# Kernel tuning notes

Hardware: AMD Instinct MI355X
Metric: run time of the kernel (lower is better)

## Reference

```python
import jax, jax.numpy as jnp
import numpy as np

N = 50000   # nodes
E = 800000  # edges per metapath
P = 3       # num_meta_paths
H = 4       # heads
D = 64      # out_size per head
IN = H * D  # in_size = 256 (required by residual g_emb.flatten(1) + h)
EPS = 1e-5
NEG_SLOPE = 0.2  # DGL GATConv leaky_relu default


def setup_inputs() -> dict:
    key = jax.random.key(0)
    ks = jax.random.split(key, 7)
    h = jax.random.normal(ks[0], (N, IN), jnp.float32)
    path_mask = jnp.ones((N, P), jnp.float32)
    src = jax.random.randint(ks[1], (P, E), 0, N, jnp.int32)
    dst = jax.random.randint(ks[2], (P, E), 0, N, jnp.int32)
    # per-metapath GATConv params (bias=False)
    fc_w = jax.random.normal(ks[3], (P, IN, H * D), jnp.float32) * 0.05
    attn_l = jax.random.normal(ks[4], (P, H, D), jnp.float32) * 0.05
    attn_r = jax.random.normal(ks[5], (P, H, D), jnp.float32) * 0.05
    bn_gamma = jnp.ones((IN,), jnp.float32)
    bn_beta = jnp.zeros((IN,), jnp.float32)
    return {"h": h, "path_mask": path_mask, "src": src, "dst": dst,
            "fc_w": fc_w, "attn_l": attn_l, "attn_r": attn_r,
            "bn_gamma": bn_gamma, "bn_beta": bn_beta}


def _gat(h, src, dst, w, al, ar):
    # DGL GATConv: linear proj, additive attention, edge-softmax over dst neighborhoods
    feat = (h @ w).reshape(N, H, D)                       # [N,H,D]
    el = jnp.sum(feat * al, axis=-1)                      # [N,H]
    er = jnp.sum(feat * ar, axis=-1)                      # [N,H]
    e = jax.nn.leaky_relu(el[src] + er[dst], NEG_SLOPE)   # [E,H]
    # numerically-stable segment softmax over incoming edges of each dst node
    m = jax.ops.segment_max(e, dst, num_segments=N)       # [N,H]
    ex = jnp.exp(e - m[dst])
    denom = jax.ops.segment_sum(ex, dst, num_segments=N)  # [N,H]
    alpha = ex / denom[dst]                               # [E,H]
    out = jax.ops.segment_sum(alpha[:, :, None] * feat[src], dst, num_segments=N)  # [N,H,D]
    return jax.nn.relu(out), alpha


def _bn(x, gamma, beta):
    # BatchNorm1d in training mode: batch statistics over node dim
    mu = jnp.mean(x, axis=0)
    var = jnp.var(x, axis=0)
    return gamma * (x - mu) * jax.lax.rsqrt(var + EPS) + beta


def reference(h, path_mask, src, dst, fc_w, attn_l, attn_r, bn_gamma, bn_beta):
    embs, attns = [], []
    for p in range(P):
        o, a = _gat(h, src[p], dst[p], fc_w[p], attn_l[p], attn_r[p])
        embs.append(_bn(o.reshape(N, H * D) + h, bn_gamma, bn_beta))
        attns.append(jnp.mean(a, axis=1))  # mean over heads -> per-edge coef [E]
    sem = jnp.stack(embs, axis=1)                              # [N,P,IN]
    w = path_mask / jnp.sum(path_mask, axis=1, keepdims=True)  # masked mean weights [N,P]
    pooled = jnp.einsum('np,npd->nd', w, sem)                  # [N,IN]
    gat_attns = jnp.stack(attns)                               # [P,E] (sparse values; indices = src/dst)
    return pooled, w, gat_attns
```

## Files before the change

### kernel.cpp

```cpp
#include <hip/hip_runtime.h>
#include <stdint.h>

#define N_NODES 50000
#define N_EDGES 800000
#define N_PATHS 3
#define N_HEADS 4
#define IN_F 256
#define BN_EPS 1e-5f
#define NEG_SLOPE 0.2f
#define CAP 48
#define NB_PER_PATH 49
#define NB_TOT (N_PATHS * NB_PER_PATH)
#define REC_CAP 18432
#define BIN_EPB 4096
#define TOT_EDGES (N_PATHS * N_EDGES)
#define BIN_BLOCKS ((TOT_EDGES + BIN_EPB - 1) / BIN_EPB)

typedef short bf16x8 __attribute__((ext_vector_type(8)));
typedef float f32x4 __attribute__((ext_vector_type(4)));

__device__ inline unsigned short f2bf(float f) {
  unsigned u = __float_as_uint(f);
  unsigned r = (u + 0x7FFFu + ((u >> 16) & 1u)) >> 16;
  return (unsigned short)r;
}
__device__ inline float bf2f(unsigned short s) {
  return __uint_as_float(((unsigned)s) << 16);
}

__global__ __launch_bounds__(256) void k_zero(unsigned* p, int nwords) {
  int i = blockIdx.x * 256 + threadIdx.x;
  if (i < nwords) p[i] = 0u;
}

__global__ __launch_bounds__(256) void k_convert_h(const float* __restrict__ h,
                                                   unsigned short* __restrict__ hbf) {
  int idx = (blockIdx.x * 256 + threadIdx.x) * 4;
  float4 v = *(const float4*)(h + idx);
  unsigned u0 = (unsigned)f2bf(v.x) | ((unsigned)f2bf(v.y) << 16);
  unsigned u1 = (unsigned)f2bf(v.z) | ((unsigned)f2bf(v.w) << 16);
  *(uint2*)(hbf + idx) = make_uint2(u0, u1);
}

__global__ __launch_bounds__(256) void k_convert_w(const float* __restrict__ fcw,
                                                   unsigned short* __restrict__ wbf) {
  __shared__ float sh[32][33];
  int bt = blockIdx.x;
  int p = bt >> 6;
  int tile = bt & 63;
  int tk = tile >> 3, tn = tile & 7;
  const float* base = fcw + (size_t)p * IN_F * IN_F;
  unsigned short* ob = wbf + (size_t)p * IN_F * IN_F;
  int c = threadIdx.x & 31, r0 = threadIdx.x >> 5;
  #pragma unroll
  for (int it = 0; it < 4; ++it) {
    int r = r0 + it * 8;
    sh[r][c] = base[(size_t)(tk * 32 + r) * IN_F + tn * 32 + c];
  }
  __syncthreads();
  #pragma unroll
  for (int it = 0; it < 4; ++it) {
    int r = r0 + it * 8;
    ob[(size_t)(tn * 32 + r) * IN_F + tk * 32 + c] = f2bf(sh[c][r]);
  }
}

__global__ __launch_bounds__(256) void k_wout(const float* __restrict__ pmask,
                                              float* __restrict__ wout) {
  int idx = blockIdx.x * 256 + threadIdx.x;
  if (idx >= N_NODES * N_PATHS) return;
  int n = idx / N_PATHS;
  float s = pmask[n * 3] + pmask[n * 3 + 1] + pmask[n * 3 + 2];
  wout[idx] = pmask[idx] / s;
}

__global__ __launch_bounds__(256) void k_bin(const int* __restrict__ src, const int* __restrict__ dst,
                                             unsigned* __restrict__ gcurP, unsigned* __restrict__ grec) {
  __shared__ unsigned hist[NB_TOT];
  __shared__ unsigned lbase[NB_TOT];
  __shared__ unsigned gbase[NB_TOT];
  __shared__ unsigned lcur[NB_TOT];
  __shared__ unsigned scanbuf[256];
  __shared__ unsigned char sbuck[BIN_EPB];
  __shared__ unsigned stage[BIN_EPB];
  int t = threadIdx.x;
  int base = blockIdx.x * BIN_EPB;
  for (int i = t; i < NB_TOT; i += 256) { hist[i] = 0u; lcur[i] = 0u; }
  __syncthreads();

  unsigned rec[16];
  int bk[16];
  #pragma unroll
  for (int k = 0; k < 16; ++k) {
    int gid = base + t + k * 256;
    bk[k] = -1;
    if (gid < TOT_EDGES) {
      int s = src[gid], d = dst[gid];
      int p = (gid >= 2 * N_EDGES) ? 2 : ((gid >= N_EDGES) ? 1 : 0);
      int b = p * NB_PER_PATH + (d >> 10);
      bk[k] = b;
      rec[k] = (unsigned)s | ((unsigned)(d & 1023) << 17);
      atomicAdd(&hist[b], 1u);
    }
  }
  __syncthreads();
  for (int i = t; i < NB_TOT; i += 256)
    gbase[i] = hist[i] ? atomicAdd(&gcurP[i * 16], hist[i]) : 0u;
  scanbuf[t] = (t < NB_TOT) ? hist[t] : 0u;
  __syncthreads();
  for (int off = 1; off < 256; off <<= 1) {
    unsigned v = (t >= off) ? scanbuf[t - off] : 0u;
    __syncthreads();
    scanbuf[t] += v;
    __syncthreads();
  }
  if (t < NB_TOT) lbase[t] = scanbuf[t] - hist[t];
  __syncthreads();
  #pragma unroll
  for (int k = 0; k < 16; ++k) {
    if (bk[k] >= 0) {
      int b = bk[k];
      unsigned pos = atomicAdd(&lcur[b], 1u) + lbase[b];
      stage[pos] = rec[k];
      sbuck[pos] = (unsigned char)b;
    }
  }
  __syncthreads();
  int nblk = TOT_EDGES - base;
  if (nblk > BIN_EPB) nblk = BIN_EPB;
  for (int i = t; i < nblk; i += 256) {
    int b = sbuck[i];
    unsigned off = (unsigned)i - lbase[b];
    unsigned gpos = gbase[b] + off;
    if (gpos < REC_CAP) grec[(size_t)b * REC_CAP + gpos] = stage[i];
  }
}

__global__ __launch_bounds__(1024) void k_fine(const unsigned* __restrict__ gcurP,
                                               const unsigned* __restrict__ grec,
                                               unsigned short* __restrict__ slots,
                                               int* __restrict__ cnt) {
  __shared__ unsigned cur[1024];
  int b = blockIdx.x;
  int p = b / NB_PER_PATH;
  int nb0 = (b % NB_PER_PATH) << 10;
  int t = threadIdx.x;
  cur[t] = 0u;
  __syncthreads();
  unsigned M = gcurP[b * 16];
  if (M > REC_CAP) M = REC_CAP;
  const unsigned* rb = grec + (size_t)b * REC_CAP;
  for (unsigned i = t; i < M; i += 1024) {
    unsigned r = rb[i];
    int node = r >> 17;
    int srcv = r & 0x1FFFF;
    unsigned pos = atomicAdd(&cur[node], 1u);
    if (pos < CAP)
      slots[((size_t)(p * N_NODES + nb0 + node)) * CAP + pos] = (unsigned short)srcv;
  }
  __syncthreads();
  int node = nb0 + t;
  if (node < N_NODES) cnt[p * N_NODES + node] = (int)cur[t];
}

__global__ __launch_bounds__(256) void k_gemm(const unsigned short* __restrict__ hbf,
                                              const unsigned short* __restrict__ wbf,
                                              const float* __restrict__ attl,
                                              const float* __restrict__ attr,
                                              unsigned short* __restrict__ featbf,
                                              float* __restrict__ el,
                                              float* __restrict__ erd) {
  __shared__ unsigned short As[64 * 264];
  __shared__ unsigned short Bs[64 * 264];
  __shared__ float sal[256];
  __shared__ float sar[256];
  int m0 = blockIdx.x * 64;
  int p = blockIdx.y;
  int tid = threadIdx.x;
  const unsigned short* wptr = wbf + (size_t)p * IN_F * IN_F;

  sal[tid] = attl[p * 256 + tid];
  sar[tid] = attr[p * 256 + tid];
  for (int i = tid; i < 2048; i += 256) {
    int r = i >> 5, g = i & 31;
    int gr = m0 + r;
    uint4 v = make_uint4(0, 0, 0, 0);
    if (gr < N_NODES) v = *(const uint4*)(hbf + (size_t)gr * IN_F + g * 8);
    *(uint4*)(&As[r * 264 + g * 8]) = v;
  }

  int wv = tid >> 6, lane = tid & 63;
  int l15 = lane & 15, quad = lane >> 4;
  const unsigned short* arow = &As[(wv * 16 + l15) * 264];
  size_t featbase = (size_t)p * N_NODES * IN_F;
  float* elp = el + (size_t)p * N_NODES * 4;
  float* erdp = erd + (size_t)p * N_NODES * 8;

  for (int c = 0; c < 4; ++c) {
    __syncthreads();
    for (int i = tid; i < 2048; i += 256) {
      int r = i >> 5, g = i & 31;
      *(uint4*)(&Bs[r * 264 + g * 8]) =
          *(const uint4*)(wptr + (size_t)(c * 64 + r) * IN_F + g * 8);
    }
    __syncthreads();

    f32x4 acc[4];
    #pragma unroll
    for (int i = 0; i < 4; ++i) acc[i] = (f32x4){0.f, 0.f, 0.f, 0.f};
    #pragma unroll
    for (int kb = 0; kb < 8; ++kb) {
      bf16x8 a = *(const bf16x8*)(arow + kb * 32 + quad * 8);
      #pragma unroll
      for (int nn = 0; nn < 4; ++nn) {
        bf16x8 b = *(const bf16x8*)(&Bs[(nn * 16 + l15) * 264 + kb * 32 + quad * 8]);
        acc[nn] = __builtin_amdgcn_mfma_f32_16x16x32_bf16(a, b, acc[nn], 0, 0, 0);
      }
    }
    #pragma unroll
    for (int nn = 0; nn < 4; ++nn)
      #pragma unroll
      for (int rg = 0; rg < 4; ++rg) {
        int grow = m0 + wv * 16 + quad * 4 + rg;
        if (grow < N_NODES)
          featbf[featbase + (size_t)grow * IN_F + c * 64 + nn * 16 + l15] = f2bf(acc[nn][rg]);
      }
    #pragma unroll
    for (int rg = 0; rg < 4; ++rg) {
      float a = 0.f, b = 0.f;
      #pragma unroll
      for (int nn = 0; nn < 4; ++nn) {
        float v = acc[nn][rg];
        int col = c * 64 + nn * 16 + l15;
        a += v * sal[col];
        b += v * sar[col];
      }
      a += __shfl_xor(a, 1); a += __shfl_xor(a, 2); a += __shfl_xor(a, 4); a += __shfl_xor(a, 8);
      b += __shfl_xor(b, 1); b += __shfl_xor(b, 2); b += __shfl_xor(b, 4); b += __shfl_xor(b, 8);
      int grow = m0 + wv * 16 + quad * 4 + rg;
      if (l15 == 0 && grow < N_NODES) {
        elp[(size_t)grow * 4 + c] = a;
        erdp[(size_t)grow * 8 + c] = b;
      }
    }
  }
}

__global__ __launch_bounds__(256) void k_gather(const int* __restrict__ cnt,
                                                const unsigned short* __restrict__ slots,
                                                const float* __restrict__ el,
                                                float* __restrict__ erd,
                                                const unsigned short* __restrict__ featbf,
                                                unsigned short* __restrict__ outbuf) {
  __shared__ float red[1024];
  __shared__ float redden[16];
  __shared__ float xs[4][CAP];
  __shared__ unsigned soff[CAP];
  int b = blockIdx.x;
  int p = b / N_NODES;
  int node = b - p * N_NODES;
  int tid = threadIdx.x;
  int w = tid >> 6, lane = tid & 63;
  int head = lane >> 4;
  int m = cnt[b];
  if (m > CAP) m = CAP;
  const float* elp = el + (size_t)p * N_NODES * 4;
  float* erdp = erd + (size_t)p * N_NODES * 8;
  const unsigned short* sl = slots + (size_t)b * CAP;
  const char* fp_ = (const char*)(featbf + (size_t)p * N_NODES * IN_F + lane * 4);

  if (tid < 4 * m) {
    int e = tid >> 2, hh = tid & 3;
    int s = (int)sl[e];
    if (hh == 0) soff[e] = (unsigned)s * (unsigned)(IN_F * 2);
    float ev = elp[s * 4 + hh] + erdp[(size_t)node * 8 + hh];
    ev = ev > 0.f ? ev : NEG_SLOPE * ev;
    xs[hh][e] = __expf(ev);
  }
  __syncthreads();

  float a0 = 0.f, a1 = 0.f, a2 = 0.f, a3 = 0.f, den = 0.f;
  int i = w;
  for (; i + 12 < m; i += 16) {
    unsigned o0 = soff[i], o1 = soff[i + 4], o2 = soff[i + 8], o3 = soff[i + 12];
    float x0 = xs[head][i], x1 = xs[head][i + 4], x2 = xs[head][i + 8], x3 = xs[head][i + 12];
    uint2 f0 = *(const uint2*)(fp_ + o0);
    uint2 f1 = *(const uint2*)(fp_ + o1);
    uint2 f2 = *(const uint2*)(fp_ + o2);
    uint2 f3 = *(const uint2*)(fp_ + o3);
    den += (x0 + x1) + (x2 + x3);
    a0 += x0 * __uint_as_float(f0.x << 16) + x1 * __uint_as_float(f1.x << 16) +
          x2 * __uint_as_float(f2.x << 16) + x3 * __uint_as_float(f3.x << 16);
    a1 += x0 * __uint_as_float(f0.x & 0xFFFF0000u) + x1 * __uint_as_float(f1.x & 0xFFFF0000u) +
          x2 * __uint_as_float(f2.x & 0xFFFF0000u) + x3 * __uint_as_float(f3.x & 0xFFFF0000u);
    a2 += x0 * __uint_as_float(f0.y << 16) + x1 * __uint_as_float(f1.y << 16) +
          x2 * __uint_as_float(f2.y << 16) + x3 * __uint_as_float(f3.y << 16);
    a3 += x0 * __uint_as_float(f0.y & 0xFFFF0000u) + x1 * __uint_as_float(f1.y & 0xFFFF0000u) +
          x2 * __uint_as_float(f2.y & 0xFFFF0000u) + x3 * __uint_as_float(f3.y & 0xFFFF0000u);
  }
  for (; i + 4 < m; i += 8) {
    unsigned o0 = soff[i], o1 = soff[i + 4];
    float x0 = xs[head][i], x1 = xs[head][i + 4];
    uint2 f0 = *(const uint2*)(fp_ + o0);
    uint2 f1 = *(const uint2*)(fp_ + o1);
    den += x0 + x1;
    a0 += x0 * __uint_as_float(f0.x << 16) + x1 * __uint_as_float(f1.x << 16);
    a1 += x0 * __uint_as_float(f0.x & 0xFFFF0000u) + x1 * __uint_as_float(f1.x & 0xFFFF0000u);
    a2 += x0 * __uint_as_float(f0.y << 16) + x1 * __uint_as_float(f1.y << 16);
    a3 += x0 * __uint_as_float(f0.y & 0xFFFF0000u) + x1 * __uint_as_float(f1.y & 0xFFFF0000u);
  }
  for (; i < m; i += 4) {
    unsigned o0 = soff[i];
    float x0 = xs[head][i];
    uint2 f = *(const uint2*)(fp_ + o0);
    den += x0;
    a0 += x0 * __uint_as_float(f.x << 16);
    a1 += x0 * __uint_as_float(f.x & 0xFFFF0000u);
    a2 += x0 * __uint_as_float(f.y << 16);
    a3 += x0 * __uint_as_float(f.y & 0xFFFF0000u);
  }
  *(float4*)&red[w * 256 + lane * 4] = make_float4(a0, a1, a2, a3);
  if ((lane & 15) == 0) redden[w * 4 + head] = den;
  __syncthreads();
  int col = tid;
  float o = red[col] + red[256 + col] + red[512 + col] + red[768 + col];
  int ht = tid >> 6;
  float dsum = redden[ht] + redden[4 + ht] + redden[8 + ht] + redden[12 + ht];
  float inv = dsum > 0.f ? 1.f / dsum : 0.f;
  o = fmaxf(o * inv, 0.f);
  outbuf[(size_t)b * IN_F + col] = f2bf(o);
  if ((tid & 63) == 0) erdp[(size_t)node * 8 + 4 + ht] = inv;
}

__global__ __launch_bounds__(256) void k_attn(const int* __restrict__ src, const int* __restrict__ dst,
                                              const float* __restrict__ el,
                                              const float* __restrict__ erd,
                                              float* __restrict__ attn_out) {
  int eid = blockIdx.x * 256 + threadIdx.x;
  int p = eid / N_EDGES;
  int s = src[eid], t = dst[eid];
  const float* elp = el + (size_t)p * N_NODES * 4;
  const float* erdp = erd + (size_t)p * N_NODES * 8;
  float4 a = *(const float4*)(elp + (size_t)s * 4);
  float4 b = *(const float4*)(erdp + (size_t)t * 8);
  float4 idn = *(const float4*)(erdp + (size_t)t * 8 + 4);
  float4 e;
  e.x = a.x + b.x; e.x = e.x > 0.f ? e.x : NEG_SLOPE * e.x;
  e.y = a.y + b.y; e.y = e.y > 0.f ? e.y : NEG_SLOPE * e.y;
  e.z = a.z + b.z; e.z = e.z > 0.f ? e.z : NEG_SLOPE * e.z;
  e.w = a.w + b.w; e.w = e.w > 0.f ? e.w : NEG_SLOPE * e.w;
  attn_out[eid] = 0.25f * (__expf(e.x) * idn.x + __expf(e.y) * idn.y +
                           __expf(e.z) * idn.z + __expf(e.w) * idn.w);
}

__global__ __launch_bounds__(256) void k_bnstats3(const unsigned short* __restrict__ outbuf,
                                                  const float* __restrict__ h,
                                                  float* __restrict__ colsum, float* __restrict__ colsq) {
  int t = threadIdx.x;
  float s0 = 0.f, q0 = 0.f, s1 = 0.f, q1 = 0.f, s2 = 0.f, q2 = 0.f;
  for (int r = blockIdx.x; r < N_NODES; r += gridDim.x) {
    float hv = h[(size_t)r * IN_F + t];
    float v0 = bf2f(outbuf[(size_t)r * IN_F + t]) + hv;
    float v1 = bf2f(outbuf[((size_t)N_NODES + r) * IN_F + t]) + hv;
    float v2 = bf2f(outbuf[((size_t)2 * N_NODES + r) * IN_F + t]) + hv;
    s0 += v0; q0 += v0 * v0;
    s1 += v1; q1 += v1 * v1;
    s2 += v2; q2 += v2 * v2;
  }
  atomicAdd(&colsum[t], s0);
  atomicAdd(&colsq[t], q0);
  atomicAdd(&colsum[256 + t], s1);
  atomicAdd(&colsq[256 + t], q1);
  atomicAdd(&colsum[512 + t], s2);
  atomicAdd(&colsq[512 + t], q2);
}

__global__ __launch_bounds__(256) void k_bnapply3(const unsigned short* __restrict__ outbuf,
                                                  const float* __restrict__ h,
                                                  const float* __restrict__ colsum, const float* __restrict__ colsq,
                                                  const float* __restrict__ gamma, const float* __restrict__ beta,
                                                  const float* __restrict__ pmask,
                                                  float* __restrict__ pooled) {
  __shared__ float spm[3];
  int n = blockIdx.x, t = threadIdx.x;
  if (t < 3) spm[t] = pmask[n * 3 + t];
  __syncthreads();
  float ssum = spm[0] + spm[1] + spm[2];
  const float invN = 1.f / (float)N_NODES;
  float hv = h[(size_t)n * IN_F + t];
  float g = gamma[t], bt = beta[t];
  float pv = 0.f;
  #pragma unroll
  for (int p = 0; p < 3; ++p) {
    float mu = colsum[p * 256 + t] * invN;
    float var = colsq[p * 256 + t] * invN - mu * mu;
    float rs = rsqrtf(var + BN_EPS);
    float v = bf2f(outbuf[((size_t)p * N_NODES + n) * IN_F + t]) + hv;
    float emb = g * (v - mu) * rs + bt;
    pv += (spm[p] / ssum) * emb;
  }
  pooled[(size_t)n * IN_F + t] = pv;
}

extern "C" void kernel_launch(void* const* d_in, const int* in_sizes, int n_in,
                              void* d_out, int out_size, void* d_ws, size_t ws_size,
                              hipStream_t stream) {
  const float* h     = (const float*)d_in[0];
  const float* pmask = (const float*)d_in[1];
  const int*   src   = (const int*)d_in[2];
  const int*   dst   = (const int*)d_in[3];
  const float* fcw   = (const float*)d_in[4];
  const float* attl  = (const float*)d_in[5];
  const float* attr  = (const float*)d_in[6];
  const float* gamma = (const float*)d_in[7];
  const float* beta  = (const float*)d_in[8];

  float* out_pooled = (float*)d_out;
  float* out_w = out_pooled + (size_t)N_NODES * IN_F;
  float* out_attn = out_w + (size_t)N_NODES * N_PATHS;

  char* wp = (char*)d_ws;
  auto carve = [&](size_t bytes) {
    char* r = wp;
    wp += (bytes + 255) & ~(size_t)255;
    return r;
  };
  unsigned short* hbf    = (unsigned short*)carve((size_t)N_NODES * IN_F * 2);
  unsigned short* featbf = (unsigned short*)carve((size_t)N_PATHS * N_NODES * IN_F * 2);
  unsigned short* wbf    = (unsigned short*)carve((size_t)N_PATHS * IN_F * IN_F * 2);
  unsigned short* outbuf = (unsigned short*)carve((size_t)N_PATHS * N_NODES * IN_F * 2);
  char* grec_base = carve((size_t)NB_TOT * REC_CAP * 4);
  unsigned* grec = (unsigned*)grec_base;
  float* el  = (float*)grec_base;
  float* erd = el + (size_t)N_PATHS * N_NODES * 4;
  unsigned short* slots = (unsigned short*)carve((size_t)N_PATHS * N_NODES * CAP * 2);
  int* cnt = (int*)carve((size_t)N_PATHS * N_NODES * 4);
  char* zbase = wp;
  unsigned* gcurP = (unsigned*)carve((size_t)NB_TOT * 16 * 4);
  float* colsum = (float*)carve((size_t)N_PATHS * IN_F * 4);
  float* colsq  = (float*)carve((size_t)N_PATHS * IN_F * 4);
  int zero_words = (int)((wp - zbase) / 4);

  k_convert_h<<<(N_NODES * IN_F) / 1024, 256, 0, stream>>>(h, hbf);
  k_convert_w<<<N_PATHS * 64, 256, 0, stream>>>(fcw, wbf);
  k_wout<<<(N_NODES * N_PATHS + 255) / 256, 256, 0, stream>>>(pmask, out_w);
  k_zero<<<(zero_words + 255) / 256, 256, 0, stream>>>((unsigned*)zbase, zero_words);
  k_bin<<<BIN_BLOCKS, 256, 0, stream>>>(src, dst, gcurP, grec);
  k_fine<<<NB_TOT, 1024, 0, stream>>>(gcurP, grec, slots, cnt);
  k_gemm<<<dim3((N_NODES + 63) / 64, N_PATHS), 256, 0, stream>>>(hbf, wbf, attl, attr,
                                                                 featbf, el, erd);
  k_gather<<<N_PATHS * N_NODES, 256, 0, stream>>>(cnt, slots, el, erd, featbf, outbuf);
  k_attn<<<TOT_EDGES / 256, 256, 0, stream>>>(src, dst, el, erd, out_attn);
  k_bnstats3<<<512, 256, 0, stream>>>(outbuf, h, colsum, colsq);
  k_bnapply3<<<N_NODES, 256, 0, stream>>>(outbuf, h, colsum, colsq, gamma, beta, pmask,
                                          out_pooled);
}
```

Baseline: 594.3 us.

## Assign one wavefront per destination node in gather kernel

The gather kernel now processes four destination nodes per block, one wavefront each, instead of one node per 256-thread block split across four waves. This removes both block-wide __syncthreads barriers and the shared-memory cross-wave reduction, and each lane writes packed bf16 output directly. In exchange each wave walks all incoming edges serially, so per-node latency grows and there is less memory-level parallelism per node. The shared-memory writes and reads within a wave also lose their explicit barrier.

```diff
diff --git a/kernel.cpp b/kernel.cpp
--- a/kernel.cpp
+++ b/kernel.cpp
@@ -252,15 +252,13 @@
                                                 float* __restrict__ erd,
                                                 const unsigned short* __restrict__ featbf,
                                                 unsigned short* __restrict__ outbuf) {
-  __shared__ float red[1024];
-  __shared__ float redden[16];
-  __shared__ float xs[4][CAP];
-  __shared__ unsigned soff[CAP];
-  int b = blockIdx.x;
-  int p = b / N_NODES;
-  int node = b - p * N_NODES;
+  __shared__ float xs[4][4][CAP];
+  __shared__ unsigned soff[4][CAP];
+  int p = blockIdx.y;
   int tid = threadIdx.x;
-  int w = tid >> 6, lane = tid & 63;
+  int wv = tid >> 6, lane = tid & 63;
+  int node = blockIdx.x * 4 + wv;
+  int b = p * N_NODES + node;
   int head = lane >> 4;
   int m = cnt[b];
   if (m > CAP) m = CAP;
@@ -269,21 +267,23 @@
   const unsigned short* sl = slots + (size_t)b * CAP;
   const char* fp_ = (const char*)(featbf + (size_t)p * N_NODES * IN_F + lane * 4);
 
-  if (tid < 4 * m) {
-    int e = tid >> 2, hh = tid & 3;
-    int s = (int)sl[e];
-    if (hh == 0) soff[e] = (unsigned)s * (unsigned)(IN_F * 2);
-    float ev = elp[s * 4 + hh] + erdp[(size_t)node * 8 + hh];
-    ev = ev > 0.f ? ev : NEG_SLOPE * ev;
-    xs[hh][e] = __expf(ev);
-  }
-  __syncthreads();
+  {
+    float ern = erdp[(size_t)node * 8 + head];
+    for (int e = lane & 15; e < m; e += 16) {
+      int s = (int)sl[e];
+      if (head == 0) soff[wv][e] = (unsigned)s * (unsigned)(IN_F * 2);
+      float ev = elp[s * 4 + head] + ern;
+      ev = ev > 0.f ? ev : NEG_SLOPE * ev;
+      xs[wv][head][e] = __expf(ev);
+    }
+  }
 
   float a0 = 0.f, a1 = 0.f, a2 = 0.f, a3 = 0.f, den = 0.f;
-  int i = w;
-  for (; i + 12 < m; i += 16) {
-    unsigned o0 = soff[i], o1 = soff[i + 4], o2 = soff[i + 8], o3 = soff[i + 12];
-    float x0 = xs[head][i], x1 = xs[head][i + 4], x2 = xs[head][i + 8], x3 = xs[head][i + 12];
+  int i = 0;
+  for (; i + 3 < m; i += 4) {
+    unsigned o0 = soff[wv][i], o1 = soff[wv][i + 1], o2 = soff[wv][i + 2], o3 = soff[wv][i + 3];
+    float x0 = xs[wv][head][i], x1 = xs[wv][head][i + 1];
+    float x2 = xs[wv][head][i + 2], x3 = xs[wv][head][i + 3];
     uint2 f0 = *(const uint2*)(fp_ + o0);
     uint2 f1 = *(const uint2*)(fp_ + o1);
     uint2 f2 = *(const uint2*)(fp_ + o2);
@@ -298,20 +298,9 @@
     a3 += x0 * __uint_as_float(f0.y & 0xFFFF0000u) + x1 * __uint_as_float(f1.y & 0xFFFF0000u) +
           x2 * __uint_as_float(f2.y & 0xFFFF0000u) + x3 * __uint_as_float(f3.y & 0xFFFF0000u);
   }
-  for (; i + 4 < m; i += 8) {
-    unsigned o0 = soff[i], o1 = soff[i + 4];
-    float x0 = xs[head][i], x1 = xs[head][i + 4];
-    uint2 f0 = *(const uint2*)(fp_ + o0);
-    uint2 f1 = *(const uint2*)(fp_ + o1);
-    den += x0 + x1;
-    a0 += x0 * __uint_as_float(f0.x << 16) + x1 * __uint_as_float(f1.x << 16);
-    a1 += x0 * __uint_as_float(f0.x & 0xFFFF0000u) + x1 * __uint_as_float(f1.x & 0xFFFF0000u);
-    a2 += x0 * __uint_as_float(f0.y << 16) + x1 * __uint_as_float(f1.y << 16);
-    a3 += x0 * __uint_as_float(f0.y & 0xFFFF0000u) + x1 * __uint_as_float(f1.y & 0xFFFF0000u);
-  }
-  for (; i < m; i += 4) {
-    unsigned o0 = soff[i];
-    float x0 = xs[head][i];
+  for (; i < m; ++i) {
+    unsigned o0 = soff[wv][i];
+    float x0 = xs[wv][head][i];
     uint2 f = *(const uint2*)(fp_ + o0);
     den += x0;
     a0 += x0 * __uint_as_float(f.x << 16);
@@ -319,17 +308,16 @@
     a2 += x0 * __uint_as_float(f.y << 16);
     a3 += x0 * __uint_as_float(f.y & 0xFFFF0000u);
   }
-  *(float4*)&red[w * 256 + lane * 4] = make_float4(a0, a1, a2, a3);
-  if ((lane & 15) == 0) redden[w * 4 + head] = den;
-  __syncthreads();
-  int col = tid;
-  float o = red[col] + red[256 + col] + red[512 + col] + red[768 + col];
-  int ht = tid >> 6;
-  float dsum = redden[ht] + redden[4 + ht] + redden[8 + ht] + redden[12 + ht];
-  float inv = dsum > 0.f ? 1.f / dsum : 0.f;
-  o = fmaxf(o * inv, 0.f);
-  outbuf[(size_t)b * IN_F + col] = f2bf(o);
-  if ((tid & 63) == 0) erdp[(size_t)node * 8 + 4 + ht] = inv;
+
+  float inv = den > 0.f ? 1.f / den : 0.f;
+  float o0 = fmaxf(a0 * inv, 0.f);
+  float o1 = fmaxf(a1 * inv, 0.f);
+  float o2 = fmaxf(a2 * inv, 0.f);
+  float o3 = fmaxf(a3 * inv, 0.f);
+  unsigned u0 = (unsigned)f2bf(o0) | ((unsigned)f2bf(o1) << 16);
+  unsigned u1 = (unsigned)f2bf(o2) | ((unsigned)f2bf(o3) << 16);
+  *(uint2*)(outbuf + (size_t)b * IN_F + lane * 4) = make_uint2(u0, u1);
+  if ((lane & 15) == 0) erdp[(size_t)node * 8 + 4 + head] = inv;
 }
 
 __global__ __launch_bounds__(256) void k_attn(const int* __restrict__ src, const int* __restrict__ dst,
@@ -449,7 +437,7 @@
   k_fine<<<NB_TOT, 1024, 0, stream>>>(gcurP, grec, slots, cnt);
   k_gemm<<<dim3((N_NODES + 63) / 64, N_PATHS), 256, 0, stream>>>(hbf, wbf, attl, attr,
                                                                  featbf, el, erd);
-  k_gather<<<N_PATHS * N_NODES, 256, 0, stream>>>(cnt, slots, el, erd, featbf, outbuf);
+  k_gather<<<dim3(N_NODES / 4, N_PATHS), 256, 0, stream>>>(cnt, slots, el, erd, featbf, outbuf);
   k_attn<<<TOT_EDGES / 256, 256, 0, stream>>>(src, dst, el, erd, out_attn);
   k_bnstats3<<<512, 256, 0, stream>>>(outbuf, h, colsum, colsq);
   k_bnapply3<<<N_NODES, 256, 0, stream>>>(outbuf, h, colsum, colsq, gamma, beta, pmask,
```

New measurement: 557.8 us. 6.1% less time.
